# Kernel tuning notes

Hardware: AMD Instinct MI355X
Metric: run time of the kernel (lower is better)

Reference implementation:

```python
import jax, jax.numpy as jnp
import numpy as np

N = 256        # ImageSize
NC = 8         # coils
NSPOKE = 34    # radial spokes
NVEC = 512     # samples per spoke
K = NSPOKE * NVEC  # total k-space points


def setup_inputs() -> dict:
    key = jax.random.key(0)
    k1, k2, k3, k4 = jax.random.split(key, 4)
    input_r = jax.random.normal(k1, (N, N, 2), dtype=jnp.float32)
    C_r = jax.random.normal(k2, (NC, N, N, 2), dtype=jnp.float32)
    w = jax.random.uniform(k3, (NVEC,), dtype=jnp.float32)
    # nonuniform k-space coordinates in [-pi, pi)
    angle = jax.random.uniform(k4, (K, 2), dtype=jnp.float32,
                               minval=-np.pi, maxval=np.pi)
    return {"input_r": input_r, "C_r": C_r, "w": w, "angle": angle}


def reference(input_r, C_r, w, angle):
    # Type-3 NUFFT: y[c,k] = sum_j C[c,j]*x[j] * exp(-i*(s_k*(-x1_j) + t_k*(-x2_j)))
    #             = sum_{a,b} (C[c,a,b]*x[a,b]) * exp(+i*s_k*g[a]) * exp(+i*t_k*g[b])
    # since the source grid is separable: x1_j = g[a], x2_j = g[b],
    # g = linspace(-N//2, N//2-1, N) for even N (iflag=0 -> negative sign).
    n = input_r.shape[0]
    nvec = w.shape[0]
    g = jnp.arange(n, dtype=jnp.float32) - n // 2          # [N]

    x = input_r[..., 0] + 1j * input_r[..., 1]             # [N,N] complex64
    C = C_r[..., 0] + 1j * C_r[..., 1]                     # [Nc,N,N] complex64
    Xc = C * x[None]                                       # coil-weighted image [Nc,N,N]

    s = angle[:, 0]                                        # [K]
    t = angle[:, 1]                                        # [K]
    E1 = jnp.exp(1j * s[:, None] * g[None, :])             # [K,N] phase along axis a
    E2 = jnp.exp(1j * t[:, None] * g[None, :])             # [K,N] phase along axis b

    # contract b first -> [Nc,K,N], then a -> [Nc,K]
    y = jnp.einsum('kb,cab,ka->ck', E2, Xc, E1, optimize=True)  # [Nc,K]

    # density compensation: wr = tile(w, (Nc, Nspoke, 1)).reshape(Nc, -1)
    wr = jnp.tile(w, y.shape[1] // nvec)                   # [K]
    y = y * wr[None, :]

    return jnp.stack([jnp.real(y), jnp.imag(y)], axis=-1)  # [Nc,K,2] float32
```

## Files before the change

kernel.cpp:

```cpp
#include <hip/hip_runtime.h>
#include <hip/hip_bf16.h>
#include <stdint.h>


#define NKTOT 17408
#define NBLK 272
#define NT 8

typedef short bf16x8 __attribute__((ext_vector_type(8)));
typedef float f32x4 __attribute__((ext_vector_type(4)));
typedef float f32x16 __attribute__((ext_vector_type(16)));

__device__ __forceinline__ unsigned short f2bf(float f) {
  unsigned int u = __builtin_bit_cast(unsigned int, f);
  u += 0x7FFFu + ((u >> 16) & 1u);
  return (unsigned short)(u >> 16);
}
__device__ __forceinline__ unsigned int pk2bf(float lo, float hi) {
  return (unsigned int)f2bf(lo) | ((unsigned int)f2bf(hi) << 16);
}

__device__ __forceinline__ size_t aidx(int c, int m, int jj) {
  int tt = jj >> 5, q = (jj >> 4) & 1, h = (jj >> 3) & 1;
  return (size_t)c * 131072 + (tt * 2 + q) * 8192 + h * 4096 + m * 8 + (jj & 7);
}

__global__ __launch_bounds__(256) void pack_a(
    const float* __restrict__ input_r, const float* __restrict__ C_r,
    unsigned short* __restrict__ Apack, float* __restrict__ biastab)
{
  const int bx = blockIdx.x;
  const int tid = threadIdx.x;
  const int p = bx * 2 + (tid >> 7);
  const int a = p & 255;
  const int c = p >> 8;
  const int j = tid & 127;
  const size_t xbase = (size_t)a * 256;
  const size_t cbase = ((size_t)(c * 256 + a)) * 256;
  if (j == 0) {
    float xr = input_r[(xbase + 128) * 2], xi = input_r[(xbase + 128) * 2 + 1];
    float cr = C_r[(cbase + 128) * 2],     ci = C_r[(cbase + 128) * 2 + 1];
    biastab[c * 512 + a]       = cr * xr - ci * xi;
    biastab[c * 512 + 256 + a] = cr * xi + ci * xr;
    xr = input_r[xbase * 2]; xi = input_r[xbase * 2 + 1];
    cr = C_r[cbase * 2];     ci = C_r[cbase * 2 + 1];
    float reb = cr * xr - ci * xi, imb = cr * xi + ci * xr;
    Apack[aidx(c, a, 127)]       = f2bf(reb);
    Apack[aidx(c, a, 255)]       = f2bf(imb);
    Apack[aidx(c, 256 + a, 127)] = f2bf(imb);
    Apack[aidx(c, 256 + a, 255)] = f2bf(-reb);
  } else {
    const int bp = 128 + j, bm = 128 - j;
    float xpr = input_r[(xbase + bp) * 2], xpi = input_r[(xbase + bp) * 2 + 1];
    float cpr = C_r[(cbase + bp) * 2],     cpi = C_r[(cbase + bp) * 2 + 1];
    float pr = cpr * xpr - cpi * xpi, pi = cpr * xpi + cpi * xpr;
    float xmr = input_r[(xbase + bm) * 2], xmi = input_r[(xbase + bm) * 2 + 1];
    float cmr = C_r[(cbase + bm) * 2],     cmi = C_r[(cbase + bm) * 2 + 1];
    float mrv = cmr * xmr - cmi * xmi, miv = cmr * xmi + cmi * xmr;
    Apack[aidx(c, a, j - 1)]         = f2bf(pr + mrv);
    Apack[aidx(c, a, 127 + j)]       = f2bf(miv - pi);
    Apack[aidx(c, 256 + a, j - 1)]   = f2bf(pi + miv);
    Apack[aidx(c, 256 + a, 127 + j)] = f2bf(pr - mrv);
  }
}

__global__ __launch_bounds__(512, 4) void gemm_fused(
    const unsigned short* __restrict__ Apack,
    const float* __restrict__ biastab,
    const float* __restrict__ angle,
    const float* __restrict__ wvec,
    float* __restrict__ out)
{
  __shared__ unsigned short Bs[64 * 256];
  __shared__ float scol[8][2][64];

  const int bx = blockIdx.x;
  const int c = (bx >> 3) & 7;
  const int ktile = (bx >> 6) * 8 + (bx & 7);
  const int kt0 = ktile * 64;
  const int tid = threadIdx.x;
  const int w = tid >> 6;
  const int l = tid & 63;
  const int l31 = l & 31;
  const int l5 = l >> 5;

  const unsigned short* Alane = Apack + (size_t)c * 131072
      + l5 * 4096 + (size_t)(w * 64 + l31) * 8;

  {
    const float t_reg = angle[(size_t)(kt0 + l) * 2 + 1];
    float2 et;
    __sincosf(t_reg, &et.y, &et.x);
    float zr, zi;
    __sincosf(t_reg * (float)((w & 3) * 32 + 1), &zi, &zr);
    const bool use_cos = (w < 4);
#pragma unroll
    for (int oc = 0; oc < 4; ++oc) {
      float v[8];
#pragma unroll
      for (int o8 = 0; o8 < 8; ++o8) {
        v[o8] = use_cos ? zr : zi;
        float nr = zr * et.x - zi * et.y;
        float ni = zr * et.y + zi * et.x;
        zr = nr; zi = ni;
      }
      uint4 pk;
      pk.x = pk2bf(v[0], v[1]);
      pk.y = pk2bf(v[2], v[3]);
      pk.z = pk2bf(v[4], v[5]);
      pk.w = pk2bf(v[6], v[7]);
      const int chunk = w * 4 + oc;
      const int pos = (chunk & 24) | ((chunk & 7) ^ (l & 7));
      *(uint4*)&Bs[l * 256 + pos * 8] = pk;
    }
  }

  f32x16 acc[2][2];
#pragma unroll
  for (int rg = 0; rg < 2; ++rg) {
#pragma unroll
    for (int q2 = 0; q2 < 4; ++q2) {
      f32x4 b4 = *(const f32x4*)(biastab + c * 512 + w * 64 + rg * 32
                                 + 4 * l5 + 8 * q2);
#pragma unroll
      for (int r2 = 0; r2 < 4; ++r2) {
        acc[rg][0][q2 * 4 + r2] = b4[r2];
        acc[rg][1][q2 * 4 + r2] = b4[r2];
      }
    }
  }
  __syncthreads();

#pragma unroll 2
  for (int tt = 0; tt < NT; ++tt) {
#pragma unroll
    for (int q = 0; q < 2; ++q) {
      const int ks = tt * 2 + q;
      bf16x8 af0 = *(const bf16x8*)(Alane + (size_t)ks * 8192);
      bf16x8 af1 = *(const bf16x8*)(Alane + (size_t)ks * 8192 + 256);
      const int chunk = ks * 2 + l5;
      const int pos8 = ((chunk & 24) | ((chunk & 7) ^ (l & 7))) * 8;
      bf16x8 bf0 = *(const bf16x8*)&Bs[l31 * 256 + pos8];
      bf16x8 bf1 = *(const bf16x8*)&Bs[(32 + l31) * 256 + pos8];
      acc[0][0] = __builtin_amdgcn_mfma_f32_32x32x16_bf16(af0, bf0, acc[0][0], 0, 0, 0);
      acc[0][1] = __builtin_amdgcn_mfma_f32_32x32x16_bf16(af0, bf1, acc[0][1], 0, 0, 0);
      acc[1][0] = __builtin_amdgcn_mfma_f32_32x32x16_bf16(af1, bf0, acc[1][0], 0, 0, 0);
      acc[1][1] = __builtin_amdgcn_mfma_f32_32x32x16_bf16(af1, bf1, acc[1][1], 0, 0, 0);
    }
  }

#pragma unroll
  for (int cg = 0; cg < 2; ++cg) {
    const int col = cg * 32 + l31;
    const int k = kt0 + col;
    const float s = angle[(size_t)k * 2];
    float s1, c1, s8, c8;
    __sincosf(s, &s1, &c1);
    __sincosf(8.f * s, &s8, &c8);
    float c2 = c1 * c1 - s1 * s1, s2 = 2.f * c1 * s1;
    float c3 = c2 * c1 - s2 * s1, s3 = c2 * s1 + s2 * c1;
    float c16 = c8 * c8 - s8 * s8, s16 = 2.f * c8 * s8;
    float c24 = c16 * c8 - s16 * s8, s24 = s16 * c8 + c16 * s8;
    const float Yr[4] = {1.f, c8, c16, c24};
    const float Yi[4] = {0.f, s8, s16, s24};
    float sumr = 0.f, sumi = 0.f;
#pragma unroll
    for (int rg = 0; rg < 2; ++rg) {
      float Or = 0.f, Oi = 0.f;
#pragma unroll
      for (int q2 = 0; q2 < 4; ++q2) {
        float v0 = acc[rg][cg][q2 * 4 + 0], v1 = acc[rg][cg][q2 * 4 + 1];
        float v2 = acc[rg][cg][q2 * 4 + 2], v3 = acc[rg][cg][q2 * 4 + 3];
        float Ir = v0 + c1 * v1 + c2 * v2 + c3 * v3;
        float Ii = s1 * v1 + s2 * v2 + s3 * v3;
        Or += Yr[q2] * Ir - Yi[q2] * Ii;
        Oi += Yi[q2] * Ir + Yr[q2] * Ii;
      }
      const float a0f = (float)((w & 3) * 64 + rg * 32 + 4 * l5 - 128);
      float sb, cb;
      __sincosf(s * a0f, &sb, &cb);
      sumr += cb * Or - sb * Oi;
      sumi += sb * Or + cb * Oi;
    }
    sumr += __shfl_xor(sumr, 32, 64);
    sumi += __shfl_xor(sumi, 32, 64);
    if (l5 == 0) {
      scol[w][0][col] = sumr;
      scol[w][1][col] = sumi;
    }
  }
  __syncthreads();
  if (tid < 128) {
    const int col = tid >> 1;
    const int comp = tid & 1;
    const int k = kt0 + col;
    float re = scol[0][0][col] + scol[1][0][col] + scol[2][0][col] + scol[3][0][col]
             - scol[4][1][col] - scol[5][1][col] - scol[6][1][col] - scol[7][1][col];
    float im = scol[0][1][col] + scol[1][1][col] + scol[2][1][col] + scol[3][1][col]
             + scol[4][0][col] + scol[5][0][col] + scol[6][0][col] + scol[7][0][col];
    float val = comp ? im : re;
    out[((size_t)c * NKTOT + k) * 2 + comp] = val * wvec[k & 511];
  }
}

extern "C" void kernel_launch(void* const* d_in, const int* in_sizes, int n_in,
                              void* d_out, int out_size, void* d_ws, size_t ws_size,
                              hipStream_t stream) {
  const float* input_r = (const float*)d_in[0];
  const float* C_r     = (const float*)d_in[1];
  const float* wvec    = (const float*)d_in[2];
  const float* angle   = (const float*)d_in[3];
  float* out = (float*)d_out;

  unsigned short* Apack = (unsigned short*)d_ws;
  float* biastab = (float*)((char*)d_ws + (size_t)2097152);

  pack_a<<<1024, 256, 0, stream>>>(input_r, C_r, Apack, biastab);
  gemm_fused<<<8 * NBLK, 512, 0, stream>>>(Apack, biastab, angle, wvec, out);
}
```

Before: 114.0 us.

## Double k-tile per block to 128 columns with 16 waves sharing A fragments

Each block now handles 128 k-points using 1024 threads arranged as 8 row-waves by 2 column-waves. The goal is to halve the number of blocks and reuse the shared-memory sin/cos B table across more work. The B-table generation also changes from a serial complex-rotation recurrence to a fresh __sincosf every 4 entries, which shortens the dependency chain but adds transcendental calls. Each block uses more shared memory and threads, which can lower occupancy, and the A fragments are now read twice per block, once by each column-wave.

```diff
diff --git a/kernel.cpp b/kernel.cpp
--- a/kernel.cpp
+++ b/kernel.cpp
@@ -4,7 +4,7 @@
 
 
 #define NKTOT 17408
-#define NBLK 272
+#define NBLK2 136
 #define NT 8
 
 typedef short bf16x8 __attribute__((ext_vector_type(8)));
@@ -64,54 +64,62 @@
   }
 }
 
-__global__ __launch_bounds__(512, 4) void gemm_fused(
+__global__ __launch_bounds__(1024, 4) void gemm_fused(
     const unsigned short* __restrict__ Apack,
     const float* __restrict__ biastab,
     const float* __restrict__ angle,
     const float* __restrict__ wvec,
     float* __restrict__ out)
 {
-  __shared__ unsigned short Bs[64 * 256];
-  __shared__ float scol[8][2][64];
+  __shared__ unsigned short Bs[128 * 256];
+  __shared__ float scol[8][2][128];
 
   const int bx = blockIdx.x;
   const int c = (bx >> 3) & 7;
   const int ktile = (bx >> 6) * 8 + (bx & 7);
-  const int kt0 = ktile * 64;
+  const int kt0 = ktile * 128;
   const int tid = threadIdx.x;
   const int w = tid >> 6;
+  const int wr = w >> 1;
+  const int wc = w & 1;
   const int l = tid & 63;
   const int l31 = l & 31;
   const int l5 = l >> 5;
 
   const unsigned short* Alane = Apack + (size_t)c * 131072
-      + l5 * 4096 + (size_t)(w * 64 + l31) * 8;
+      + l5 * 4096 + (size_t)(wr * 64 + l31) * 8;
 
   {
-    const float t_reg = angle[(size_t)(kt0 + l) * 2 + 1];
+    const int r = tid & 127;
+    const int cq = tid >> 7;
+    const float t_reg = angle[(size_t)(kt0 + r) * 2 + 1];
     float2 et;
     __sincosf(t_reg, &et.y, &et.x);
-    float zr, zi;
-    __sincosf(t_reg * (float)((w & 3) * 32 + 1), &zi, &zr);
-    const bool use_cos = (w < 4);
+    const bool use_cos = (cq < 4);
+    const int jbase = (cq & 3) * 32 + 1;
 #pragma unroll
     for (int oc = 0; oc < 4; ++oc) {
       float v[8];
 #pragma unroll
-      for (int o8 = 0; o8 < 8; ++o8) {
-        v[o8] = use_cos ? zr : zi;
-        float nr = zr * et.x - zi * et.y;
-        float ni = zr * et.y + zi * et.x;
-        zr = nr; zi = ni;
+      for (int half = 0; half < 2; ++half) {
+        float s0, c0;
+        __sincosf(t_reg * (float)(jbase + oc * 8 + half * 4), &s0, &c0);
+        float c1 = c0 * et.x - s0 * et.y, s1 = s0 * et.x + c0 * et.y;
+        float c2 = c1 * et.x - s1 * et.y, s2 = s1 * et.x + c1 * et.y;
+        float c3 = c2 * et.x - s2 * et.y, s3 = s2 * et.x + c2 * et.y;
+        v[half * 4 + 0] = use_cos ? c0 : s0;
+        v[half * 4 + 1] = use_cos ? c1 : s1;
+        v[half * 4 + 2] = use_cos ? c2 : s2;
+        v[half * 4 + 3] = use_cos ? c3 : s3;
       }
       uint4 pk;
       pk.x = pk2bf(v[0], v[1]);
       pk.y = pk2bf(v[2], v[3]);
       pk.z = pk2bf(v[4], v[5]);
       pk.w = pk2bf(v[6], v[7]);
-      const int chunk = w * 4 + oc;
-      const int pos = (chunk & 24) | ((chunk & 7) ^ (l & 7));
-      *(uint4*)&Bs[l * 256 + pos * 8] = pk;
+      const int chunk = cq * 4 + oc;
+      const int pos = (chunk & 24) | ((chunk & 7) ^ (r & 7));
+      *(uint4*)&Bs[r * 256 + pos * 8] = pk;
     }
   }
 
@@ -120,7 +128,7 @@
   for (int rg = 0; rg < 2; ++rg) {
 #pragma unroll
     for (int q2 = 0; q2 < 4; ++q2) {
-      f32x4 b4 = *(const f32x4*)(biastab + c * 512 + w * 64 + rg * 32
+      f32x4 b4 = *(const f32x4*)(biastab + c * 512 + wr * 64 + rg * 32
                                  + 4 * l5 + 8 * q2);
 #pragma unroll
       for (int r2 = 0; r2 < 4; ++r2) {
@@ -131,6 +139,7 @@
   }
   __syncthreads();
 
+  const int brow0 = (wc * 64 + l31) * 256;
 #pragma unroll 2
   for (int tt = 0; tt < NT; ++tt) {
 #pragma unroll
@@ -140,8 +149,8 @@
       bf16x8 af1 = *(const bf16x8*)(Alane + (size_t)ks * 8192 + 256);
       const int chunk = ks * 2 + l5;
       const int pos8 = ((chunk & 24) | ((chunk & 7) ^ (l & 7))) * 8;
-      bf16x8 bf0 = *(const bf16x8*)&Bs[l31 * 256 + pos8];
-      bf16x8 bf1 = *(const bf16x8*)&Bs[(32 + l31) * 256 + pos8];
+      bf16x8 bf0 = *(const bf16x8*)&Bs[brow0 + pos8];
+      bf16x8 bf1 = *(const bf16x8*)&Bs[brow0 + 32 * 256 + pos8];
       acc[0][0] = __builtin_amdgcn_mfma_f32_32x32x16_bf16(af0, bf0, acc[0][0], 0, 0, 0);
       acc[0][1] = __builtin_amdgcn_mfma_f32_32x32x16_bf16(af0, bf1, acc[0][1], 0, 0, 0);
       acc[1][0] = __builtin_amdgcn_mfma_f32_32x32x16_bf16(af1, bf0, acc[1][0], 0, 0, 0);
@@ -151,18 +160,18 @@
 
 #pragma unroll
   for (int cg = 0; cg < 2; ++cg) {
-    const int col = cg * 32 + l31;
+    const int col = wc * 64 + cg * 32 + l31;
     const int k = kt0 + col;
     const float s = angle[(size_t)k * 2];
-    float s1, c1, s8, c8;
+    float s1, c1, sY, cY;
     __sincosf(s, &s1, &c1);
-    __sincosf(8.f * s, &s8, &c8);
+    __sincosf(8.f * s, &sY, &cY);
     float c2 = c1 * c1 - s1 * s1, s2 = 2.f * c1 * s1;
     float c3 = c2 * c1 - s2 * s1, s3 = c2 * s1 + s2 * c1;
-    float c16 = c8 * c8 - s8 * s8, s16 = 2.f * c8 * s8;
-    float c24 = c16 * c8 - s16 * s8, s24 = s16 * c8 + c16 * s8;
-    const float Yr[4] = {1.f, c8, c16, c24};
-    const float Yi[4] = {0.f, s8, s16, s24};
+    float cY2 = cY * cY - sY * sY, sY2 = 2.f * cY * sY;
+    float cY3 = cY2 * cY - sY2 * sY, sY3 = cY2 * sY + sY2 * cY;
+    const float Yr[4] = {1.f, cY, cY2, cY3};
+    const float Yi[4] = {0.f, sY, sY2, sY3};
     float sumr = 0.f, sumi = 0.f;
 #pragma unroll
     for (int rg = 0; rg < 2; ++rg) {
@@ -176,7 +185,7 @@
         Or += Yr[q2] * Ir - Yi[q2] * Ii;
         Oi += Yi[q2] * Ir + Yr[q2] * Ii;
       }
-      const float a0f = (float)((w & 3) * 64 + rg * 32 + 4 * l5 - 128);
+      const float a0f = (float)((wr & 3) * 64 + rg * 32 + 4 * l5 - 128);
       float sb, cb;
       __sincosf(s * a0f, &sb, &cb);
       sumr += cb * Or - sb * Oi;
@@ -185,12 +194,12 @@
     sumr += __shfl_xor(sumr, 32, 64);
     sumi += __shfl_xor(sumi, 32, 64);
     if (l5 == 0) {
-      scol[w][0][col] = sumr;
-      scol[w][1][col] = sumi;
+      scol[wr][0][col] = sumr;
+      scol[wr][1][col] = sumi;
     }
   }
   __syncthreads();
-  if (tid < 128) {
+  if (tid < 256) {
     const int col = tid >> 1;
     const int comp = tid & 1;
     const int k = kt0 + col;
@@ -216,5 +225,5 @@
   float* biastab = (float*)((char*)d_ws + (size_t)2097152);
 
   pack_a<<<1024, 256, 0, stream>>>(input_r, C_r, Apack, biastab);
-  gemm_fused<<<8 * NBLK, 512, 0, stream>>>(Apack, biastab, angle, wvec, out);
-}
+  gemm_fused<<<8 * NBLK2, 1024, 0, stream>>>(Apack, biastab, angle, wvec, out);
+}
```

Result: slower. 117.3 us (+2.9%).
